# Performance work log

Hardware: AMD Instinct MI355X
Metric: run time of the kernel (lower is better)

Reference implementation:

```python
import jax, jax.numpy as jnp
import numpy as np

D_MODEL = 1024
N_HEADS = 16
D_HEAD = D_MODEL // N_HEADS  # 64
M = int(round(D_HEAD * np.log(D_HEAD)))  # 266 random features, per source
KERNEL_EPS = 1e-4


def setup_inputs() -> dict:
    key = jax.random.key(0)
    ks = jax.random.split(key, 12)
    B, L = 2, 2048
    sc = 1.0 / np.sqrt(D_MODEL)
    return {
        "query": jax.random.normal(ks[0], (B, L, D_MODEL), jnp.float32),
        "key_": jax.random.normal(ks[1], (B, L, D_MODEL), jnp.float32),
        "value": jax.random.normal(ks[2], (B, L, D_MODEL), jnp.float32),
        "Wq": jax.random.normal(ks[3], (D_MODEL, D_MODEL), jnp.float32) * sc,
        "bq": jnp.zeros((D_MODEL,), jnp.float32),
        "Wk": jax.random.normal(ks[4], (D_MODEL, D_MODEL), jnp.float32) * sc,
        "bk": jnp.zeros((D_MODEL,), jnp.float32),
        "Wv": jax.random.normal(ks[5], (D_MODEL, D_MODEL), jnp.float32) * sc,
        "bv": jnp.zeros((D_MODEL,), jnp.float32),
        "Wo": jax.random.normal(ks[6], (D_MODEL, D_MODEL), jnp.float32) * sc,
        "bo": jnp.zeros((D_MODEL,), jnp.float32),
        "random_features": jax.random.normal(ks[7], (M, D_HEAD), jnp.float32),
    }


def _split_heads(x):
    # [B,L,d_model] -> [B,H,L,D]
    B, L, _ = x.shape
    return x.reshape(B, L, N_HEADS, D_HEAD).transpose(0, 2, 1, 3)


def _favor_projected(q, k, rf):
    # q,k: [B,H,L,D]; rf: [M,D]. Faithful to get_projected_queries_and_keys (kernel_type='exp').
    q = q / (D_MODEL ** 0.25)
    k = k / (D_MODEL ** 0.25)
    pq = jnp.einsum('bhld,md->bhlm', q, rf)
    pk = jnp.einsum('bhld,md->bhlm', k, rf)
    h_q = -0.5 * jnp.sum(q * q, axis=-1, keepdims=True)  # [B,H,L,1]
    h_k = -0.5 * jnp.sum(k * k, axis=-1, keepdims=True)
    q_stab = jnp.max(h_q, axis=-1, keepdims=True)  # == h_q (last dim is 1), as in source
    k_stab = jnp.max(h_k)  # global scalar, as in source
    q_ker = jnp.exp(h_q + (pq - q_stab))
    k_ker = jnp.exp(h_k + (pk - k_stab))
    c = M ** (-0.5)
    return c * (q_ker + KERNEL_EPS), c * (k_ker + KERNEL_EPS)


def _causal_favor(qp, kp, v):
    # qp,kp: [L,B,H,M]; v: [L,B,H,D]. Prefix-sum linear attention.
    # Denominator: q_prime[i] . cumsum(k_prime)[i]
    denom = jnp.einsum('lbhm,lbhm->lbh', qp, jnp.cumsum(kp, axis=0))

    # Numerator: recurrent scan carrying S = sum_j k'_j v_j^T  ([B,H,M,D])
    def step(S, inp):
        q_t, k_t, v_t = inp
        S = S + k_t[..., :, None] * v_t[..., None, :]
        out_t = jnp.einsum('bhmd,bhm->bhd', S, q_t)
        return S, out_t

    S0 = jnp.zeros(kp.shape[1:] + (v.shape[-1],), kp.dtype)
    _, num = jax.lax.scan(step, S0, (qp, kp, v))  # num: [L,B,H,D]
    return num / denom[..., None]


def reference(query, key_, value, Wq, bq, Wk, bk, Wv, bv, Wo, bo, random_features):
    B, L, _ = query.shape
    q = _split_heads(query @ Wq + bq)   # [B,H,L,D]
    k = _split_heads(key_ @ Wk + bk)
    v = _split_heads(value @ Wv + bv)
    q_prime, k_prime = _favor_projected(q, k, random_features)  # [B,H,L,M]
    # Causal path operates sequence-first: [L,B,H,*]
    qp = q_prime.transpose(2, 0, 1, 3)
    kp = k_prime.transpose(2, 0, 1, 3)
    vt = v.transpose(2, 0, 1, 3)
    out = _causal_favor(qp, kp, vt)               # [L,B,H,D]
    ctx = out.transpose(1, 0, 2, 3).reshape(B, L, D_MODEL)
    return ctx @ Wo + bo
```

## Files before the change

kernel.cpp:

```cpp
#include <hip/hip_runtime.h>
#include <hip/hip_bf16.h>

#define BATCH 2
#define SEQ 2048
#define DMODEL 1024
#define NH 16
#define HD 64
#define NRF 266
#define NRFP 288
#define SROW 320
#define CHK 128
#define NCH 16
#define NBH 32
#define NROWS 4096

constexpr float SCAL = 0.17677669529663687f;
constexpr float SCAL2 = 0.03125f;
constexpr float LN_CNORM = -2.7917480361965505f;
constexpr float CKEPS = 6.131393094576169e-6f;

typedef short bf16x8 __attribute__((ext_vector_type(8)));
typedef float f32x4 __attribute__((ext_vector_type(4)));

__device__ __forceinline__ short f2bs(float v) {
  __hip_bfloat16 h = __float2bfloat16(v);
  return *reinterpret_cast<short*>(&h);
}
__device__ __forceinline__ float bs2f(short s) {
  __hip_bfloat16 h;
  *reinterpret_cast<short*>(&h) = s;
  return __bfloat162float(h);
}
__device__ __forceinline__ void gload_lds16(const void* g, void* l) {
  __builtin_amdgcn_global_load_lds(
      (const __attribute__((address_space(1))) void*)g,
      (__attribute__((address_space(3))) void*)l, 16, 0, 0);
}
__device__ __forceinline__ unsigned f2ord(float f) {
  unsigned u = __float_as_uint(f);
  return (u & 0x80000000u) ? ~u : (u | 0x80000000u);
}
__device__ __forceinline__ float ord2f(unsigned e) {
  return (e & 0x80000000u) ? __uint_as_float(e & 0x7fffffffu)
                           : __uint_as_float(~e);
}

__global__ __launch_bounds__(256) void cvt3_kernel(const float* __restrict__ q,
                                                   const float* __restrict__ k,
                                                   const float* __restrict__ v,
                                                   short* __restrict__ out) {
  int z = blockIdx.y;
  const float* x = (z == 0) ? q : (z == 1) ? k : v;
  short* y = out + (size_t)z * NROWS * DMODEL;
  int i = (blockIdx.x * 256 + threadIdx.x) * 8;
  float4 a = *(const float4*)&x[i];
  float4 b = *(const float4*)&x[i + 4];
  bf16x8 o;
  o[0] = f2bs(a.x); o[1] = f2bs(a.y); o[2] = f2bs(a.z); o[3] = f2bs(a.w);
  o[4] = f2bs(b.x); o[5] = f2bs(b.y); o[6] = f2bs(b.z); o[7] = f2bs(b.w);
  *(bf16x8*)&y[i] = o;
}

__global__ __launch_bounds__(256) void rf_pad_bf16(const float* __restrict__ rf,
                                                   short* __restrict__ rfb,
                                                   unsigned* __restrict__ kord) {
  int idx = blockIdx.x * 256 + threadIdx.x;
  rfb[idx] = (idx < NRF * HD) ? f2bs(rf[idx] * SCAL) : (short)0;
  if (idx == 0) *kord = 0u;
}

__global__ __launch_bounds__(256) void transpose4_bf16(
    const float* __restrict__ Wq, const float* __restrict__ Wk,
    const float* __restrict__ Wv, const float* __restrict__ Wo,
    short* __restrict__ WtBase) {
  __shared__ float t[32][33];
  int z = blockIdx.z;
  const float* W = (z == 0) ? Wq : (z == 1) ? Wk : (z == 2) ? Wv : Wo;
  short* Wt = WtBase + (size_t)z * DMODEL * DMODEL;
  int k0 = blockIdx.y << 5, n0 = blockIdx.x << 5;
  int tx = threadIdx.x & 31, ty = threadIdx.x >> 5;
#pragma unroll
  for (int rr = 0; rr < 4; ++rr) {
    int r = ty + (rr << 3);
    t[r][tx] = W[(size_t)(k0 + r) * DMODEL + n0 + tx];
  }
  __syncthreads();
#pragma unroll
  for (int rr = 0; rr < 4; ++rr) {
    int r = ty + (rr << 3);
    Wt[(size_t)(n0 + r) * DMODEL + k0 + tx] = f2bs(t[tx][r]);
  }
}

template <bool OUTBF>
__device__ __forceinline__ void gemm_core128(const short* __restrict__ A,
                                             const short* __restrict__ Bt,
                                             const float* __restrict__ bias,
                                             void* __restrict__ C, int bm, int bn) {
  __shared__ short As[2][128 * 64];
  __shared__ short Bs[2][128 * 64];
  int tid = threadIdx.x;
  int lane = tid & 63, wid = tid >> 6;
  int wr = wid >> 1, wc = wid & 1;
  int cl = lane & 15, rq = lane >> 4;
  f32x4 acc[4][4];
#pragma unroll
  for (int m = 0; m < 4; ++m)
#pragma unroll
    for (int n = 0; n < 4; ++n) acc[m][n] = f32x4{0.f, 0.f, 0.f, 0.f};

  auto stage = [&](int buf, int k0) {
#pragma unroll
    for (int i = 0; i < 4; ++i) {
      int e = tid * 8 + i * 2048;
      int row = e >> 6;
      int k = (e & 63) ^ ((row & 7) << 3);
      gload_lds16(A + (size_t)(bm + row) * DMODEL + k0 + k,
                  &As[buf][wid * 512 + i * 2048]);
    }
#pragma unroll
    for (int i = 0; i < 4; ++i) {
      int e = tid * 8 + i * 2048;
      int row = e >> 6;
      int k = (e & 63) ^ ((row & 7) << 3);
      gload_lds16(Bt + (size_t)(bn + row) * DMODEL + k0 + k,
                  &Bs[buf][wid * 512 + i * 2048]);
    }
  };

  stage(0, 0);
#pragma unroll 2
  for (int t = 0; t < 16; ++t) {
    int cur = t & 1;
    if (t < 15) {
      stage(cur ^ 1, (t + 1) * 64);
      asm volatile("s_waitcnt vmcnt(8)" ::: "memory");
    } else {
      asm volatile("s_waitcnt vmcnt(0)" ::: "memory");
    }
    __builtin_amdgcn_s_barrier();
    asm volatile("" ::: "memory");
    const short* curA = &As[cur][0];
    const short* curB = &Bs[cur][0];
#pragma unroll
    for (int ks = 0; ks < 2; ++ks) {
      int kb = ks * 32 + (rq << 3);
      bf16x8 af[4], bfv[4];
#pragma unroll
      for (int mf = 0; mf < 4; ++mf) {
        int row = wr * 64 + mf * 16 + cl;
        af[mf] = *(const bf16x8*)&curA[row * 64 + (kb ^ ((row & 7) << 3))];
      }
#pragma unroll
      for (int nf = 0; nf < 4; ++nf) {
        int row = wc * 64 + nf * 16 + cl;
        bfv[nf] = *(const bf16x8*)&curB[row * 64 + (kb ^ ((row & 7) << 3))];
      }
#pragma unroll
      for (int mf = 0; mf < 4; ++mf)
#pragma unroll
        for (int nf = 0; nf < 4; ++nf)
          acc[mf][nf] = __builtin_amdgcn_mfma_f32_16x16x32_bf16(af[mf], bfv[nf],
                                                                acc[mf][nf], 0, 0, 0);
    }
    __builtin_amdgcn_s_barrier();
    asm volatile("" ::: "memory");
  }
  int rbase = bm + wr * 64 + (rq << 2);
  int cbase = bn + wc * 64 + cl;
#pragma unroll
  for (int nf = 0; nf < 4; ++nf) {
    int col = cbase + nf * 16;
    float bv = bias[col];
#pragma unroll
    for (int mf = 0; mf < 4; ++mf)
#pragma unroll
      for (int r = 0; r < 4; ++r) {
        int row = rbase + mf * 16 + r;
        float v = acc[mf][nf][r] + bv;
        if (OUTBF)
          ((short*)C)[(size_t)row * DMODEL + col] = f2bs(v);
        else
          ((float*)C)[(size_t)row * DMODEL + col] = v;
      }
  }
}

template <bool OUTBF>
__device__ __forceinline__ void gemm_core64(const short* __restrict__ A,
                                            const short* __restrict__ Bt,
                                            const float* __restrict__ bias,
                                            void* __restrict__ C, int bm, int bn) {
  __shared__ short As[2][128 * 64];
  __shared__ short Bs[2][64 * 64];
  int tid = threadIdx.x;
  int lane = tid & 63, wid = tid >> 6;
  int wr = wid >> 1, wc = wid & 1;
  f32x4 acc[4][2];
#pragma unroll
  for (int m = 0; m < 4; ++m)
#pragma unroll
    for (int n = 0; n < 2; ++n) acc[m][n] = f32x4{0.f, 0.f, 0.f, 0.f};

  auto stage = [&](int buf, int k0) {
#pragma unroll
    for (int i = 0; i < 4; ++i) {
      int e = tid * 8 + i * 2048;
      int row = e >> 6;
      int k = (e & 63) ^ ((row & 7) << 3);
      gload_lds16(A + (size_t)(bm + row) * DMODEL + k0 + k,
                  &As[buf][wid * 512 + i * 2048]);
    }
#pragma unroll
    for (int i = 0; i < 2; ++i) {
      int e = tid * 8 + i * 2048;
      int row = e >> 6;
      int k = (e & 63) ^ ((row & 7) << 3);
      gload_lds16(Bt + (size_t)(bn + row) * DMODEL + k0 + k,
                  &Bs[buf][wid * 512 + i * 2048]);
    }
  };

  stage(0, 0);
#pragma unroll 2
  for (int t = 0; t < 16; ++t) {
    int cur = t & 1;
    if (t < 15) {
      stage(cur ^ 1, (t + 1) * 64);
      asm volatile("s_waitcnt vmcnt(6)" ::: "memory");
    } else {
      asm volatile("s_waitcnt vmcnt(0)" ::: "memory");
    }
    __builtin_amdgcn_s_barrier();
    asm volatile("" ::: "memory");
    const short* curA = &As[cur][0];
    const short* curB = &Bs[cur][0];
#pragma unroll
    for (int ks = 0; ks < 2; ++ks) {
      int kb = ks * 32 + ((lane >> 4) << 3);
      bf16x8 af[4], bfv[2];
#pragma unroll
      for (int mf = 0; mf < 4; ++mf) {
        int row = wr * 64 + mf * 16 + (lane & 15);
        af[mf] = *(const bf16x8*)&curA[row * 64 + (kb ^ ((row & 7) << 3))];
      }
#pragma unroll
      for (int nf = 0; nf < 2; ++nf) {
        int row = wc * 32 + nf * 16 + (lane & 15);
        bfv[nf] = *(const bf16x8*)&curB[row * 64 + (kb ^ ((row & 7) << 3))];
      }
#pragma unroll
      for (int mf = 0; mf < 4; ++mf)
#pragma unroll
        for (int nf = 0; nf < 2; ++nf)
          acc[mf][nf] = __builtin_amdgcn_mfma_f32_16x16x32_bf16(af[mf], bfv[nf],
                                                                acc[mf][nf], 0, 0, 0);
    }
    __builtin_amdgcn_s_barrier();
    asm volatile("" ::: "memory");
  }
  int rbase = bm + wr * 64 + ((lane >> 4) << 2);
  int cbase = bn + wc * 32 + (lane & 15);
#pragma unroll
  for (int nf = 0; nf < 2; ++nf) {
    int col = cbase + nf * 16;
    float bv = bias[col];
#pragma unroll
    for (int mf = 0; mf < 4; ++mf)
#pragma unroll
      for (int r = 0; r < 4; ++r) {
        int row = rbase + mf * 16 + r;
        float v = acc[mf][nf][r] + bv;
        if (OUTBF)
          ((short*)C)[(size_t)row * DMODEL + col] = f2bs(v);
        else
          ((float*)C)[(size_t)row * DMODEL + col] = v;
      }
  }
}

__global__ __launch_bounds__(256) void gemm_qkv3(
    const short* __restrict__ Abase, const short* __restrict__ WtBase,
    const float* __restrict__ bq, const float* __restrict__ bk,
    const float* __restrict__ bv, short* __restrict__ OutBase) {
  int z = blockIdx.z;
  const short* A = Abase + (size_t)z * NROWS * DMODEL;
  const short* Bt = WtBase + (size_t)z * DMODEL * DMODEL;
  const float* bias = (z == 0) ? bq : (z == 1) ? bk : bv;
  short* C = OutBase + (size_t)z * NROWS * DMODEL;
  int bid = blockIdx.x + (blockIdx.y << 3);
  int swz = ((bid & 7) << 5) + (bid >> 3);
  int bn = (swz & 7) << 7;
  int bm = (swz >> 3) << 7;
  gemm_core128<true>(A, Bt, bias, C, bm, bn);
}

__global__ __launch_bounds__(256) void gemm_out(const short* __restrict__ A,
                                                const short* __restrict__ Bt,
                                                const float* __restrict__ bias,
                                                float* __restrict__ C) {
  int bid = blockIdx.x + (blockIdx.y << 4);
  int swz = ((bid & 7) << 6) + (bid >> 3);
  int bn = (swz & 15) << 6;
  int bm = (swz >> 4) << 7;
  gemm_core64<false>(A, Bt, bias, C, bm, bn);
}

__global__ __launch_bounds__(256) void hk_kernel(const short* __restrict__ Kb,
                                                 float* __restrict__ hkbuf,
                                                 unsigned* __restrict__ kord) {
  int tid = threadIdx.x;
  int rloc = tid >> 4, h = tid & 15;
  int n = blockIdx.x * 16 + rloc;
  const short* p = Kb + (size_t)n * DMODEL + h * HD;
  float ss = 0.f;
#pragma unroll
  for (int g = 0; g < 8; ++g) {
    bf16x8 v = *(const bf16x8*)(p + g * 8);
#pragma unroll
    for (int e = 0; e < 8; ++e) {
      float x = bs2f(v[e]);
      ss += x * x;
    }
  }
  float hkv = -0.5f * SCAL2 * ss;
  int b = n >> 11, l = n & (SEQ - 1);
  hkbuf[((size_t)(b * NH + h)) * SEQ + l] = hkv;
  __shared__ float red[256];
  red[tid] = hkv;
  __syncthreads();
  for (int s = 128; s > 0; s >>= 1) {
    if (tid < s) red[tid] = fmaxf(red[tid], red[tid + s]);
    __syncthreads();
  }
  if (tid == 0) atomicMax(kord, f2ord(red[0]));
}

__global__ __launch_bounds__(256, 1) void featmap_mfma(
    const short* __restrict__ Qproj, const short* __restrict__ Kproj,
    const short* __restrict__ rfb, const float* __restrict__ hkbuf,
    const unsigned* __restrict__ kord, short* __restrict__ Qp,
    short* __restrict__ Kp) {
  __shared__ short smem[26624];
  __shared__ float hks[128];
  short* As = smem;
  short* Bs = smem + 8192;
  int isK = blockIdx.z;
  const short* X = isK ? Kproj : Qproj;
  short* O = isK ? Kp : Qp;
  int bh = blockIdx.y, b = bh >> 4, h = bh & 15;
  int l0 = blockIdx.x << 7;
  int tid = threadIdx.x, lane = tid & 63, wid = tid >> 6;
  int cl = lane & 15, rq = lane >> 4;

#pragma unroll
  for (int i = 0; i < 4; ++i) {
    int e = tid * 8 + i * 2048;
    int row = e >> 6;
    int k = (e & 63) ^ ((row & 7) << 3);
    gload_lds16(X + ((size_t)b * SEQ + l0 + row) * DMODEL + h * HD + k,
                &As[wid * 512 + i * 2048]);
  }
#pragma unroll
  for (int i = 0; i < 9; ++i) {
    int e = tid * 8 + i * 2048;
    int row = e >> 6;
    int k = (e & 63) ^ ((row & 7) << 3);
    gload_lds16(rfb + row * HD + k, &Bs[wid * 512 + i * 2048]);
  }
  if (isK) {
    float ksv = ord2f(*kord);
    if (tid < 128)
      hks[tid] = hkbuf[(size_t)bh * SEQ + l0 + tid] - ksv + LN_CNORM;
  }
  __syncthreads();

  int i0 = wid * 32;
  f32x4 acc[2][18];
#pragma unroll
  for (int m = 0; m < 2; ++m)
#pragma unroll
    for (int n = 0; n < 18; ++n) acc[m][n] = f32x4{0.f, 0.f, 0.f, 0.f};
#pragma unroll
  for (int ks = 0; ks < 2; ++ks) {
    int kb = ks * 32 + (rq << 3);
    int swz = (cl & 7) << 3;
    bf16x8 af[2];
#pragma unroll
    for (int mf = 0; mf < 2; ++mf) {
      int row = i0 + mf * 16 + cl;
      af[mf] = *(const bf16x8*)&As[row * 64 + (kb ^ swz)];
    }
#pragma unroll
    for (int nf = 0; nf < 18; ++nf) {
      int brow = nf * 16 + cl;
      bf16x8 bv = *(const bf16x8*)&Bs[brow * 64 + (kb ^ swz)];
#pragma unroll
      for (int mf = 0; mf < 2; ++mf)
        acc[mf][nf] = __builtin_amdgcn_mfma_f32_16x16x32_bf16(af[mf], bv,
                                                              acc[mf][nf], 0, 0, 0);
    }
  }

  short* Ps = smem;
#pragma unroll
  for (int hf = 0; hf < 2; ++hf) {
    __syncthreads();
#pragma unroll
    for (int mf = 0; mf < 2; ++mf)
#pragma unroll
      for (int r = 0; r < 4; ++r) {
        int rl = i0 + mf * 16 + (rq << 2) + r;
        float addk = isK ? hks[rl] : LN_CNORM;
#pragma unroll
        for (int nf2 = 0; nf2 < 9; ++nf2) {
          int m = hf * 144 + nf2 * 16 + cl;
          float v = acc[mf][hf * 9 + nf2][r] + addk;
          float o = (m < NRF) ? (__expf(v) + CKEPS) : 0.f;
          Ps[rl * 152 + nf2 * 16 + cl] = f2bs(o);
        }
      }
    __syncthreads();
#pragma unroll
    for (int it = 0; it < 9; ++it) {
      int idx = tid + it * 256;
      int row = idx / 18, ch = idx - row * 18;
      bf16x8 val = *(const bf16x8*)&Ps[row * 152 + ch * 8];
      *(bf16x8*)&O[((size_t)bh * SEQ + l0 + row) * NRFP + hf * 144 + ch * 8] = val;
    }
  }
}

__global__ __launch_bounds__(256) void chunksum_mfma(
    const short* __restrict__ Kp, const short* __restrict__ Vb,
    short* __restrict__ Sct, float* __restrict__ ksum) {
  constexpr int ST = 70;
  __shared__ short KT[NRFP * ST];
  __shared__ short VT[HD * ST];
  int c = blockIdx.x, bh = blockIdx.y;
  int b = bh >> 4, h = bh & 15;
  int tid = threadIdx.x, lane = tid & 63, wv = tid >> 6;
  int cl = lane & 15, rq = lane >> 4;
  int irow = tid >> 2;
  int mq = tid & 3;
  size_t rowb = (size_t)bh * SEQ + (size_t)c * CHK;

  f32x4 acc[18];
#pragma unroll
  for (int m = 0; m < 18; ++m) acc[m] = f32x4{0.f, 0.f, 0.f, 0.f};
  float k1 = 0.f, k2 = 0.f;

  for (int hf = 0; hf < 2; ++hf) {
    __syncthreads();
    const short* Krow = Kp + (rowb + hf * 64 + irow) * NRFP;
#pragma unroll
    for (int cg = 0; cg < 9; ++cg) {
      int m0 = cg * 32 + mq * 8;
      bf16x8 v = *(const bf16x8*)(Krow + m0);
#pragma unroll
      for (int e = 0; e < 8; ++e) KT[(m0 + e) * ST + irow] = v[e];
    }
    const short* Vrow =
        Vb + ((size_t)b * SEQ + (size_t)c * CHK + hf * 64 + irow) * DMODEL + h * HD;
    {
      int d0 = mq * 16;
      bf16x8 v0 = *(const bf16x8*)(Vrow + d0);
      bf16x8 v1 = *(const bf16x8*)(Vrow + d0 + 8);
#pragma unroll
      for (int e = 0; e < 8; ++e) VT[(d0 + e) * ST + irow] = v0[e];
#pragma unroll
      for (int e = 0; e < 8; ++e) VT[(d0 + 8 + e) * ST + irow] = v1[e];
    }
    __syncthreads();
#pragma unroll
    for (int ks = 0; ks < 2; ++ks) {
      int kb = ks * 32 + rq * 8;
      bf16x8 bv = *(const bf16x8*)&VT[(wv * 16 + cl) * ST + kb];
#pragma unroll
      for (int mf = 0; mf < 18; ++mf) {
        bf16x8 av = *(const bf16x8*)&KT[(mf * 16 + cl) * ST + kb];
        acc[mf] = __builtin_amdgcn_mfma_f32_16x16x32_bf16(av, bv, acc[mf], 0, 0, 0);
      }
    }
    {
      const short* r1 = &KT[tid * ST];
#pragma unroll
      for (int g = 0; g < 8; ++g) {
        bf16x8 v = *(const bf16x8*)(r1 + g * 8);
#pragma unroll
        for (int e = 0; e < 8; ++e) k1 += bs2f(v[e]);
      }
      if (tid < 10) {
        const short* r2 = &KT[(256 + tid) * ST];
#pragma unroll
        for (int g = 0; g < 8; ++g) {
          bf16x8 v = *(const bf16x8*)(r2 + g * 8);
#pragma unroll
          for (int e = 0; e < 8; ++e) k2 += bs2f(v[e]);
        }
      }
    }
  }
  size_t sbase = ((size_t)bh * NCH + c) * (size_t)(HD * SROW);
  int d = wv * 16 + cl;
#pragma unroll
  for (int mf = 0; mf < 18; ++mf) {
    short4 o4 = make_short4(f2bs(acc[mf][0]), f2bs(acc[mf][1]),
                            f2bs(acc[mf][2]), f2bs(acc[mf][3]));
    *(short4*)&Sct[sbase + (size_t)d * SROW + mf * 16 + rq * 4] = o4;
  }
  {
    int dz = tid >> 2, off = NRFP + ((tid & 3) << 3);
    bf16x8 z = {0, 0, 0, 0, 0, 0, 0, 0};
    *(bf16x8*)&Sct[sbase + (size_t)dz * SROW + off] = z;
  }
  size_t kbase = ((size_t)bh * NCH + c) * (size_t)NRF;
  if (tid < NRF) ksum[kbase + tid] = k1;
  if (tid < 10) ksum[kbase + 256 + tid] = k2;
}

__global__ __launch_bounds__(256) void prefix_all(const short* __restrict__ Sct,
                                                  short* __restrict__ Spt,
                                                  const float* __restrict__ ksum,
                                                  short* __restrict__ ksb) {
  int bh = blockIdx.y;
  if (blockIdx.x == 80) {
    for (int m = threadIdx.x; m < NRFP; m += 256) {
      if (m < NRF) {
        size_t base = (size_t)bh * NCH * NRF + m;
        float a = 0.f;
#pragma unroll
        for (int c = 0; c < NCH; ++c) {
          float v = ksum[base + (size_t)c * NRF];
          ksb[((size_t)bh * NCH + c) * NRFP + m] = f2bs(a);
          a += v;
        }
      } else {
#pragma unroll
        for (int c = 0; c < NCH; ++c)
          ksb[((size_t)bh * NCH + c) * NRFP + m] = 0;
      }
    }
    return;
  }
  int e = blockIdx.x * 256 + threadIdx.x;
  float a = 0.f;
#pragma unroll
  for (int c = 0; c < NCH; ++c) {
    size_t idx = ((size_t)bh * NCH + c) * (size_t)(HD * SROW) + e;
    float v = bs2f(Sct[idx]);
    Spt[idx] = f2bs(a);
    a += v;
  }
}

__global__ __launch_bounds__(256) void attn_mfma(
    const short* __restrict__ Qp, const short* __restrict__ Kp,
    const short* __restrict__ Vb, const short* __restrict__ Spt,
    const short* __restrict__ ksb, short* __restrict__ ctxb) {
  constexpr int PST = 136;
  __shared__ short Vt[64 * PST];
  __shared__ short SP[64 * SROW];
  int c = blockIdx.x, bh = blockIdx.y;
  int b = bh >> 4, h = bh & 15;
  int tid = threadIdx.x, lane = tid & 63, wid = tid >> 6;
  int cl = lane & 15, rq = lane >> 4;
  size_t rowb = (size_t)bh * SEQ + (size_t)c * CHK;

  const short* sg = Spt + ((size_t)bh * NCH + c) * (size_t)(HD * SROW);
#pragma unroll
  for (int i = 0; i < 10; ++i) {
    int o = tid * 8 + i * 2048;
    int d = o / SROW;
    int m = o - d * SROW;
    int ms = m ^ ((d & 7) << 3);
    gload_lds16(sg + (size_t)d * SROW + ms, &SP[wid * 512 + i * 2048]);
  }
  {
    int jj = tid >> 3, d0 = (tid & 7) << 3;
#pragma unroll
    for (int jt = 0; jt < 4; ++jt) {
      int j = jj + jt * 32;
      bf16x8 v = *(const bf16x8*)(Vb + ((size_t)b * SEQ + (size_t)c * CHK + j) * DMODEL +
                                  h * HD + d0);
#pragma unroll
      for (int e = 0; e < 8; ++e) Vt[(d0 + e) * PST + j] = v[e];
    }
  }
  __syncthreads();

  int i0 = wid * 32;
  const short* Arow = Qp + (rowb + i0) * NRFP;
  const short* Krow = Kp + rowb * NRFP;
  const short* krow = ksb + ((size_t)bh * NCH + c) * NRFP;
  f32x4 accI[2][4];
  f32x4 accD[2];
  f32x4 accP[2][8];
#pragma unroll
  for (int m = 0; m < 2; ++m) {
#pragma unroll
    for (int n = 0; n < 4; ++n) accI[m][n] = f32x4{0.f, 0.f, 0.f, 0.f};
    accD[m] = f32x4{0.f, 0.f, 0.f, 0.f};
#pragma unroll
    for (int n = 0; n < 8; ++n) accP[m][n] = f32x4{0.f, 0.f, 0.f, 0.f};
  }
#pragma unroll
  for (int k9 = 0; k9 < 9; ++k9) {
    int kb = k9 * 32 + (rq << 3);
    bf16x8 af[2];
#pragma unroll
    for (int mf = 0; mf < 2; ++mf)
      af[mf] = *(const bf16x8*)(Arow + (size_t)(mf * 16 + cl) * NRFP + kb);
    bf16x8 bvD = {0, 0, 0, 0, 0, 0, 0, 0};
    if (cl == 0) bvD = *(const bf16x8*)(krow + kb);
#pragma unroll
    for (int mf = 0; mf < 2; ++mf)
      accD[mf] = __builtin_amdgcn_mfma_f32_16x16x32_bf16(af[mf], bvD, accD[mf], 0, 0, 0);
#pragma unroll
    for (int nf = 0; nf < 4; ++nf) {
      int row = nf * 16 + cl;
      bf16x8 bv = *(const bf16x8*)&SP[row * SROW + (kb ^ ((cl & 7) << 3))];
#pragma unroll
      for (int mf = 0; mf < 2; ++mf)
        accI[mf][nf] = __builtin_amdgcn_mfma_f32_16x16x32_bf16(af[mf], bv,
                                                               accI[mf][nf], 0, 0, 0);
    }
#pragma unroll
    for (int nf = 0; nf < 8; ++nf) {
      bf16x8 bv = *(const bf16x8*)(Krow + (size_t)(nf * 16 + cl) * NRFP + kb);
#pragma unroll
      for (int mf = 0; mf < 2; ++mf)
        accP[mf][nf] = __builtin_amdgcn_mfma_f32_16x16x32_bf16(af[mf], bv,
                                                               accP[mf][nf], 0, 0, 0);
    }
  }
  __syncthreads();

  float dtot[2][4];
#pragma unroll
  for (int mf = 0; mf < 2; ++mf)
#pragma unroll
    for (int r = 0; r < 4; ++r) {
      int rl = mf * 16 + (rq << 2) + r;
      int row = i0 + rl;
      float dsum = 0.f;
#pragma unroll
      for (int nf = 0; nf < 8; ++nf) {
        int col = nf * 16 + cl;
        float v = (col > row) ? 0.f : accP[mf][nf][r];
        dsum += v;
        SP[wid * 32 * PST + rl * PST + col] = f2bs(v);
      }
      dsum += __shfl_xor(dsum, 1);
      dsum += __shfl_xor(dsum, 2);
      dsum += __shfl_xor(dsum, 4);
      dsum += __shfl_xor(dsum, 8);
      float dden = __shfl(accD[mf][r], lane & 48);
      dtot[mf][r] = dden + dsum;
    }
  __syncthreads();

  f32x4 pacc[2][4];
#pragma unroll
  for (int m = 0; m < 2; ++m)
#pragma unroll
    for (int n = 0; n < 4; ++n) pacc[m][n] = f32x4{0.f, 0.f, 0.f, 0.f};
#pragma unroll
  for (int kk = 0; kk < 4; ++kk) {
    int kb = kk * 32 + (rq << 3);
    bf16x8 paf[2];
#pragma unroll
    for (int mf = 0; mf < 2; ++mf)
      paf[mf] = *(const bf16x8*)&SP[wid * 32 * PST + (mf * 16 + cl) * PST + kb];
#pragma unroll
    for (int nf = 0; nf < 4; ++nf) {
      bf16x8 bv = *(const bf16x8*)&Vt[(nf * 16 + cl) * PST + kb];
#pragma unroll
      for (int mf = 0; mf < 2; ++mf)
        pacc[mf][nf] = __builtin_amdgcn_mfma_f32_16x16x32_bf16(paf[mf], bv,
                                                               pacc[mf][nf], 0, 0, 0);
    }
  }
#pragma unroll
  for (int mf = 0; mf < 2; ++mf)
#pragma unroll
    for (int r = 0; r < 4; ++r) {
      int row = i0 + mf * 16 + (rq << 2) + r;
      float inv = 1.0f / dtot[mf][r];
      size_t ob = ((size_t)b * SEQ + (size_t)c * CHK + row) * DMODEL + h * HD;
#pragma unroll
      for (int nf = 0; nf < 4; ++nf) {
        int d = nf * 16 + cl;
        float v = (accI[mf][nf][r] + pacc[mf][nf][r]) * inv;
        ctxb[ob + d] = f2bs(v);
      }
    }
}

extern "C" void kernel_launch(void* const* d_in, const int* in_sizes, int n_in,
                              void* d_out, int out_size, void* d_ws, size_t ws_size,
                              hipStream_t stream) {
  (void)in_sizes; (void)n_in; (void)out_size;
  const float* query = (const float*)d_in[0];
  const float* key_  = (const float*)d_in[1];
  const float* value = (const float*)d_in[2];
  const float* Wq = (const float*)d_in[3];
  const float* bq = (const float*)d_in[4];
  const float* Wk = (const float*)d_in[5];
  const float* bk = (const float*)d_in[6];
  const float* Wv = (const float*)d_in[7];
  const float* bv = (const float*)d_in[8];
  const float* Wo = (const float*)d_in[9];
  const float* bo = (const float*)d_in[10];
  const float* rf = (const float*)d_in[11];

  constexpr size_t SZ_INBF = (size_t)NROWS * DMODEL * 2;
  constexpr size_t SZ_QP   = (size_t)NBH * SEQ * NRFP * 2;
  constexpr size_t SZ_WT   = (size_t)DMODEL * DMODEL * 2;
  constexpr size_t SZ_SCH  = (size_t)NBH * NCH * HD * SROW * 2;
  constexpr size_t SZ_KS   = (size_t)NBH * NCH * NRF * 4;
  constexpr size_t SZ_KSB  = (size_t)NBH * NCH * NRFP * 2;
  constexpr size_t SZ_HK   = (size_t)NBH * SEQ * 4;
  constexpr size_t SZ_RFB  = (size_t)NRFP * HD * 2;

  constexpr size_t O_QP   = 0;
  constexpr size_t O_KP   = O_QP + SZ_QP;
  constexpr size_t O_WT   = O_KP + SZ_QP;
  constexpr size_t O_QPR  = O_WT + 4 * SZ_WT;
  constexpr size_t O_SCH  = O_QPR + 3 * SZ_INBF;
  constexpr size_t O_SPR  = O_SCH + SZ_SCH;
  constexpr size_t O_KSUM = O_SPR + SZ_SCH;
  constexpr size_t O_KSB  = O_KSUM + SZ_KS;
  constexpr size_t O_HK   = O_KSB + SZ_KSB;
  constexpr size_t O_KST  = O_HK + SZ_HK;
  constexpr size_t O_CTXB = O_KST + 256;
  constexpr size_t O_RFB  = O_CTXB + SZ_INBF;
  constexpr size_t O_END  = O_RFB + SZ_RFB;
  if (ws_size < O_END) return;

  char* w = (char*)d_ws;
  short* Qbf  = (short*)(w + O_QP);
  short* Qp   = (short*)(w + O_QP);
  short* Kp   = (short*)(w + O_KP);
  short* WtB  = (short*)(w + O_WT);
  short* QprB = (short*)(w + O_QPR);
  short* Kpr  = (short*)(w + O_QPR + SZ_INBF);
  short* Vpr  = (short*)(w + O_QPR + 2 * SZ_INBF);
  short* Sct  = (short*)(w + O_SCH);
  short* Spt  = (short*)(w + O_SPR);
  float* ksum = (float*)(w + O_KSUM);
  short* ksb  = (short*)(w + O_KSB);
  float* hkbuf = (float*)(w + O_HK);
  unsigned* kord = (unsigned*)(w + O_KST);
  short* ctxb = (short*)(w + O_CTXB);
  short* rfb  = (short*)(w + O_RFB);

  constexpr int NEL = NROWS * DMODEL;
  cvt3_kernel<<<dim3(NEL / 2048, 3), 256, 0, stream>>>(query, key_, value, Qbf);
  transpose4_bf16<<<dim3(32, 32, 4), 256, 0, stream>>>(Wq, Wk, Wv, Wo, WtB);
  rf_pad_bf16<<<(NRFP * HD) / 256, 256, 0, stream>>>(rf, rfb, kord);
  gemm_qkv3<<<dim3(8, 32, 3), 256, 0, stream>>>(Qbf, WtB, bq, bk, bv, QprB);
  hk_kernel<<<256, 256, 0, stream>>>(Kpr, hkbuf, kord);
  featmap_mfma<<<dim3(SEQ / 128, NBH, 2), 256, 0, stream>>>(QprB, Kpr, rfb, hkbuf,
                                                            kord, Qp, Kp);
  chunksum_mfma<<<dim3(NCH, NBH), 256, 0, stream>>>(Kp, Vpr, Sct, ksum);
  prefix_all<<<dim3(81, NBH), 256, 0, stream>>>(Sct, Spt, ksum, ksb);
  attn_mfma<<<dim3(NCH, NBH), 256, 0, stream>>>(Qp, Kp, Vpr, Spt, ksb, ctxb);
  gemm_out<<<dim3(16, 32), 256, 0, stream>>>(ctxb, WtB + 3 * (size_t)DMODEL * DMODEL,
                                             bo, (float*)d_out);
}
```

Measured before the change: 184.1 us.

## Split attention chunk across two blocks and read prefix state from global

The attention kernel now launches two blocks per chunk, each handling 64 query rows, so the grid doubles from 512 to 1024 blocks and occupancy rises. The upper half skips the causally masked key columns and only computes 64 of the 128 intra-chunk columns. The prefix state is no longer staged into LDS with a swizzle but read directly from global memory per fragment, which lowers LDS use but adds uncached global traffic. Each wave now owns 16 rows instead of 32, so fewer registers are held but operand reuse across row fragments is lost.

Result: slower. 191.0 us (+3.8%).

```diff
diff --git a/kernel.cpp b/kernel.cpp
--- a/kernel.cpp
+++ b/kernel.cpp
@@ -554,147 +554,128 @@
   }
 }
 
+template <int Z>
+__device__ __forceinline__ void attn_body(short* smem, const short* __restrict__ Qp,
+                                          const short* __restrict__ Kp,
+                                          const short* __restrict__ Vb,
+                                          const short* __restrict__ Spt,
+                                          const short* __restrict__ ksb,
+                                          short* __restrict__ ctxb, int c, int bh) {
+  constexpr int JN = Z ? 128 : 64;
+  constexpr int PST = Z ? 136 : 72;
+  constexpr int NPF = Z ? 8 : 4;
+  constexpr int KK = Z ? 4 : 2;
+  short* Vt = smem;
+  short* Pl = smem + 64 * PST;
+  int b = bh >> 4, h = bh & 15;
+  int tid = threadIdx.x, lane = tid & 63, wid = tid >> 6;
+  int cl = lane & 15, rq = lane >> 4;
+  size_t rowb = (size_t)bh * SEQ + (size_t)c * CHK;
+
+  {
+    int jj = tid >> 3, d0 = (tid & 7) << 3;
+#pragma unroll
+    for (int jt = 0; jt < JN / 32; ++jt) {
+      int j = jj + jt * 32;
+      bf16x8 v = *(const bf16x8*)(Vb + ((size_t)b * SEQ + (size_t)c * CHK + j) * DMODEL +
+                                  h * HD + d0);
+#pragma unroll
+      for (int e = 0; e < 8; ++e) Vt[(d0 + e) * PST + j] = v[e];
+    }
+  }
+  __syncthreads();
+
+  int i0 = Z * 64 + wid * 16;
+  const short* Arow = Qp + (rowb + i0) * NRFP;
+  const short* Krow = Kp + rowb * NRFP;
+  const short* SptG = Spt + ((size_t)bh * NCH + c) * (size_t)(HD * SROW);
+  const short* krow = ksb + ((size_t)bh * NCH + c) * NRFP;
+  f32x4 accI[4];
+  f32x4 accD = f32x4{0.f, 0.f, 0.f, 0.f};
+  f32x4 accP[NPF];
+#pragma unroll
+  for (int n = 0; n < 4; ++n) accI[n] = f32x4{0.f, 0.f, 0.f, 0.f};
+#pragma unroll
+  for (int n = 0; n < NPF; ++n) accP[n] = f32x4{0.f, 0.f, 0.f, 0.f};
+
+#pragma unroll
+  for (int k9 = 0; k9 < 9; ++k9) {
+    int kb = k9 * 32 + (rq << 3);
+    bf16x8 af = *(const bf16x8*)(Arow + (size_t)cl * NRFP + kb);
+    bf16x8 bvD = {0, 0, 0, 0, 0, 0, 0, 0};
+    if (cl == 0) bvD = *(const bf16x8*)(krow + kb);
+    accD = __builtin_amdgcn_mfma_f32_16x16x32_bf16(af, bvD, accD, 0, 0, 0);
+#pragma unroll
+    for (int nf = 0; nf < 4; ++nf) {
+      bf16x8 bv = *(const bf16x8*)(SptG + (size_t)(nf * 16 + cl) * SROW + kb);
+      accI[nf] = __builtin_amdgcn_mfma_f32_16x16x32_bf16(af, bv, accI[nf], 0, 0, 0);
+    }
+#pragma unroll
+    for (int nf = 0; nf < NPF; ++nf) {
+      bf16x8 bv = *(const bf16x8*)(Krow + (size_t)(nf * 16 + cl) * NRFP + kb);
+      accP[nf] = __builtin_amdgcn_mfma_f32_16x16x32_bf16(af, bv, accP[nf], 0, 0, 0);
+    }
+  }
+
+  float dtot[4];
+#pragma unroll
+  for (int r = 0; r < 4; ++r) {
+    int rl = (rq << 2) + r;
+    int rowc = i0 + rl;
+    int rowl = wid * 16 + rl;
+    float dsum = 0.f;
+#pragma unroll
+    for (int nf = 0; nf < NPF; ++nf) {
+      int col = nf * 16 + cl;
+      float v = (col > rowc) ? 0.f : accP[nf][r];
+      dsum += v;
+      Pl[rowl * PST + col] = f2bs(v);
+    }
+    dsum += __shfl_xor(dsum, 1);
+    dsum += __shfl_xor(dsum, 2);
+    dsum += __shfl_xor(dsum, 4);
+    dsum += __shfl_xor(dsum, 8);
+    float dden = __shfl(accD[r], lane & 48);
+    dtot[r] = dden + dsum;
+  }
+  __syncthreads();
+
+  f32x4 pacc[4];
+#pragma unroll
+  for (int n = 0; n < 4; ++n) pacc[n] = f32x4{0.f, 0.f, 0.f, 0.f};
+#pragma unroll
+  for (int kk = 0; kk < KK; ++kk) {
+    int kb = kk * 32 + (rq << 3);
+    bf16x8 paf = *(const bf16x8*)&Pl[(wid * 16 + cl) * PST + kb];
+#pragma unroll
+    for (int nf = 0; nf < 4; ++nf) {
+      bf16x8 bv = *(const bf16x8*)&Vt[(nf * 16 + cl) * PST + kb];
+      pacc[nf] = __builtin_amdgcn_mfma_f32_16x16x32_bf16(paf, bv, pacc[nf], 0, 0, 0);
+    }
+  }
+#pragma unroll
+  for (int r = 0; r < 4; ++r) {
+    int rowc = i0 + (rq << 2) + r;
+    float inv = 1.0f / dtot[r];
+    size_t ob = ((size_t)b * SEQ + (size_t)c * CHK + rowc) * DMODEL + h * HD;
+#pragma unroll
+    for (int nf = 0; nf < 4; ++nf) {
+      int d = nf * 16 + cl;
+      ctxb[ob + d] = f2bs((accI[nf][r] + pacc[nf][r]) * inv);
+    }
+  }
+}
+
 __global__ __launch_bounds__(256) void attn_mfma(
     const short* __restrict__ Qp, const short* __restrict__ Kp,
     const short* __restrict__ Vb, const short* __restrict__ Spt,
     const short* __restrict__ ksb, short* __restrict__ ctxb) {
-  constexpr int PST = 136;
-  __shared__ short Vt[64 * PST];
-  __shared__ short SP[64 * SROW];
+  __shared__ short smem[2 * 64 * 136];
   int c = blockIdx.x, bh = blockIdx.y;
-  int b = bh >> 4, h = bh & 15;
-  int tid = threadIdx.x, lane = tid & 63, wid = tid >> 6;
-  int cl = lane & 15, rq = lane >> 4;
-  size_t rowb = (size_t)bh * SEQ + (size_t)c * CHK;
-
-  const short* sg = Spt + ((size_t)bh * NCH + c) * (size_t)(HD * SROW);
-#pragma unroll
-  for (int i = 0; i < 10; ++i) {
-    int o = tid * 8 + i * 2048;
-    int d = o / SROW;
-    int m = o - d * SROW;
-    int ms = m ^ ((d & 7) << 3);
-    gload_lds16(sg + (size_t)d * SROW + ms, &SP[wid * 512 + i * 2048]);
-  }
-  {
-    int jj = tid >> 3, d0 = (tid & 7) << 3;
-#pragma unroll
-    for (int jt = 0; jt < 4; ++jt) {
-      int j = jj + jt * 32;
-      bf16x8 v = *(const bf16x8*)(Vb + ((size_t)b * SEQ + (size_t)c * CHK + j) * DMODEL +
-                                  h * HD + d0);
-#pragma unroll
-      for (int e = 0; e < 8; ++e) Vt[(d0 + e) * PST + j] = v[e];
-    }
-  }
-  __syncthreads();
-
-  int i0 = wid * 32;
-  const short* Arow = Qp + (rowb + i0) * NRFP;
-  const short* Krow = Kp + rowb * NRFP;
-  const short* krow = ksb + ((size_t)bh * NCH + c) * NRFP;
-  f32x4 accI[2][4];
-  f32x4 accD[2];
-  f32x4 accP[2][8];
-#pragma unroll
-  for (int m = 0; m < 2; ++m) {
-#pragma unroll
-    for (int n = 0; n < 4; ++n) accI[m][n] = f32x4{0.f, 0.f, 0.f, 0.f};
-    accD[m] = f32x4{0.f, 0.f, 0.f, 0.f};
-#pragma unroll
-    for (int n = 0; n < 8; ++n) accP[m][n] = f32x4{0.f, 0.f, 0.f, 0.f};
-  }
-#pragma unroll
-  for (int k9 = 0; k9 < 9; ++k9) {
-    int kb = k9 * 32 + (rq << 3);
-    bf16x8 af[2];
-#pragma unroll
-    for (int mf = 0; mf < 2; ++mf)
-      af[mf] = *(const bf16x8*)(Arow + (size_t)(mf * 16 + cl) * NRFP + kb);
-    bf16x8 bvD = {0, 0, 0, 0, 0, 0, 0, 0};
-    if (cl == 0) bvD = *(const bf16x8*)(krow + kb);
-#pragma unroll
-    for (int mf = 0; mf < 2; ++mf)
-      accD[mf] = __builtin_amdgcn_mfma_f32_16x16x32_bf16(af[mf], bvD, accD[mf], 0, 0, 0);
-#pragma unroll
-    for (int nf = 0; nf < 4; ++nf) {
-      int row = nf * 16 + cl;
-      bf16x8 bv = *(const bf16x8*)&SP[row * SROW + (kb ^ ((cl & 7) << 3))];
-#pragma unroll
-      for (int mf = 0; mf < 2; ++mf)
-        accI[mf][nf] = __builtin_amdgcn_mfma_f32_16x16x32_bf16(af[mf], bv,
-                                                               accI[mf][nf], 0, 0, 0);
-    }
-#pragma unroll
-    for (int nf = 0; nf < 8; ++nf) {
-      bf16x8 bv = *(const bf16x8*)(Krow + (size_t)(nf * 16 + cl) * NRFP + kb);
-#pragma unroll
-      for (int mf = 0; mf < 2; ++mf)
-        accP[mf][nf] = __builtin_amdgcn_mfma_f32_16x16x32_bf16(af[mf], bv,
-                                                               accP[mf][nf], 0, 0, 0);
-    }
-  }
-  __syncthreads();
-
-  float dtot[2][4];
-#pragma unroll
-  for (int mf = 0; mf < 2; ++mf)
-#pragma unroll
-    for (int r = 0; r < 4; ++r) {
-      int rl = mf * 16 + (rq << 2) + r;
-      int row = i0 + rl;
-      float dsum = 0.f;
-#pragma unroll
-      for (int nf = 0; nf < 8; ++nf) {
-        int col = nf * 16 + cl;
-        float v = (col > row) ? 0.f : accP[mf][nf][r];
-        dsum += v;
-        SP[wid * 32 * PST + rl * PST + col] = f2bs(v);
-      }
-      dsum += __shfl_xor(dsum, 1);
-      dsum += __shfl_xor(dsum, 2);
-      dsum += __shfl_xor(dsum, 4);
-      dsum += __shfl_xor(dsum, 8);
-      float dden = __shfl(accD[mf][r], lane & 48);
-      dtot[mf][r] = dden + dsum;
-    }
-  __syncthreads();
-
-  f32x4 pacc[2][4];
-#pragma unroll
-  for (int m = 0; m < 2; ++m)
-#pragma unroll
-    for (int n = 0; n < 4; ++n) pacc[m][n] = f32x4{0.f, 0.f, 0.f, 0.f};
-#pragma unroll
-  for (int kk = 0; kk < 4; ++kk) {
-    int kb = kk * 32 + (rq << 3);
-    bf16x8 paf[2];
-#pragma unroll
-    for (int mf = 0; mf < 2; ++mf)
-      paf[mf] = *(const bf16x8*)&SP[wid * 32 * PST + (mf * 16 + cl) * PST + kb];
-#pragma unroll
-    for (int nf = 0; nf < 4; ++nf) {
-      bf16x8 bv = *(const bf16x8*)&Vt[(nf * 16 + cl) * PST + kb];
-#pragma unroll
-      for (int mf = 0; mf < 2; ++mf)
-        pacc[mf][nf] = __builtin_amdgcn_mfma_f32_16x16x32_bf16(paf[mf], bv,
-                                                               pacc[mf][nf], 0, 0, 0);
-    }
-  }
-#pragma unroll
-  for (int mf = 0; mf < 2; ++mf)
-#pragma unroll
-    for (int r = 0; r < 4; ++r) {
-      int row = i0 + mf * 16 + (rq << 2) + r;
-      float inv = 1.0f / dtot[mf][r];
-      size_t ob = ((size_t)b * SEQ + (size_t)c * CHK + row) * DMODEL + h * HD;
-#pragma unroll
-      for (int nf = 0; nf < 4; ++nf) {
-        int d = nf * 16 + cl;
-        float v = (accI[mf][nf][r] + pacc[mf][nf][r]) * inv;
-        ctxb[ob + d] = f2bs(v);
-      }
-    }
+  if (blockIdx.z == 0)
+    attn_body<0>(smem, Qp, Kp, Vb, Spt, ksb, ctxb, c, bh);
+  else
+    attn_body<1>(smem, Qp, Kp, Vb, Spt, ksb, ctxb, c, bh);
 }
 
 extern "C" void kernel_launch(void* const* d_in, const int* in_sizes, int n_in,
@@ -765,7 +746,7 @@
                                                             kord, Qp, Kp);
   chunksum_mfma<<<dim3(NCH, NBH), 256, 0, stream>>>(Kp, Vpr, Sct, ksum);
   prefix_all<<<dim3(81, NBH), 256, 0, stream>>>(Sct, Spt, ksum, ksb);
-  attn_mfma<<<dim3(NCH, NBH), 256, 0, stream>>>(Qp, Kp, Vpr, Spt, ksb, ctxb);
+  attn_mfma<<<dim3(NCH, NBH, 2), 256, 0, stream>>>(Qp, Kp, Vpr, Spt, ksb, ctxb);
   gemm_out<<<dim3(16, 32), 256, 0, stream>>>(ctxb, WtB + 3 * (size_t)DMODEL * DMODEL,
                                              bo, (float*)d_out);
 }
```

## Double-buffer K-prime tiles in LDS for the intra-chunk attention MFMA loop

Applied to the files above, without the earlier changes.

The attention kernel previously read K-prime B-operand fragments for the intra-chunk QK^T product directly from global memory, with all four waves fetching the same rows. These reads are replaced with a double-buffered LDS staging scheme: async global-to-LDS loads of 128x32 tiles with an XOR swizzle, prefetch of the next k-slice, vmcnt waits and barriers each iteration. The V transpose load is moved ahead of the S-prefix load so the waits line up. This aims to cut redundant global traffic and hide latency, at the cost of extra LDS, two barriers per iteration and a loop that is no longer fully unrolled.

After: 171.3 us. -7.0%, faster.

```diff
diff --git a/kernel.cpp b/kernel.cpp
--- a/kernel.cpp
+++ b/kernel.cpp
@@ -561,12 +561,24 @@
   constexpr int PST = 136;
   __shared__ short Vt[64 * PST];
   __shared__ short SP[64 * SROW];
+  __shared__ short Kb2[2][128 * 32];
   int c = blockIdx.x, bh = blockIdx.y;
   int b = bh >> 4, h = bh & 15;
   int tid = threadIdx.x, lane = tid & 63, wid = tid >> 6;
   int cl = lane & 15, rq = lane >> 4;
   size_t rowb = (size_t)bh * SEQ + (size_t)c * CHK;
 
+  {
+    int jj = tid >> 3, d0 = (tid & 7) << 3;
+#pragma unroll
+    for (int jt = 0; jt < 4; ++jt) {
+      int j = jj + jt * 32;
+      bf16x8 v = *(const bf16x8*)(Vb + ((size_t)b * SEQ + (size_t)c * CHK + j) * DMODEL +
+                                  h * HD + d0);
+#pragma unroll
+      for (int e = 0; e < 8; ++e) Vt[(d0 + e) * PST + j] = v[e];
+    }
+  }
   const short* sg = Spt + ((size_t)bh * NCH + c) * (size_t)(HD * SROW);
 #pragma unroll
   for (int i = 0; i < 10; ++i) {
@@ -576,22 +588,21 @@
     int ms = m ^ ((d & 7) << 3);
     gload_lds16(sg + (size_t)d * SROW + ms, &SP[wid * 512 + i * 2048]);
   }
-  {
-    int jj = tid >> 3, d0 = (tid & 7) << 3;
-#pragma unroll
-    for (int jt = 0; jt < 4; ++jt) {
-      int j = jj + jt * 32;
-      bf16x8 v = *(const bf16x8*)(Vb + ((size_t)b * SEQ + (size_t)c * CHK + j) * DMODEL +
-                                  h * HD + d0);
-#pragma unroll
-      for (int e = 0; e < 8; ++e) Vt[(d0 + e) * PST + j] = v[e];
-    }
-  }
-  __syncthreads();
+  const short* Kbase = Kp + rowb * NRFP;
+  auto stageK = [&](int buf, int k0) {
+#pragma unroll
+    for (int i = 0; i < 2; ++i) {
+      int chunk = tid + i * 256;
+      int row = chunk >> 2, cc = chunk & 3;
+      int col = k0 + ((cc ^ (row & 3)) << 3);
+      gload_lds16(Kbase + (size_t)row * NRFP + col,
+                  &Kb2[buf][(wid * 64 + i * 256) * 8]);
+    }
+  };
+  stageK(0, 0);
 
   int i0 = wid * 32;
   const short* Arow = Qp + (rowb + i0) * NRFP;
-  const short* Krow = Kp + rowb * NRFP;
   const short* krow = ksb + ((size_t)bh * NCH + c) * NRFP;
   f32x4 accI[2][4];
   f32x4 accD[2];
@@ -604,8 +615,16 @@
 #pragma unroll
     for (int n = 0; n < 8; ++n) accP[m][n] = f32x4{0.f, 0.f, 0.f, 0.f};
   }
-#pragma unroll
   for (int k9 = 0; k9 < 9; ++k9) {
+    int cur = k9 & 1;
+    if (k9 < 8) {
+      stageK(cur ^ 1, (k9 + 1) * 32);
+      asm volatile("s_waitcnt vmcnt(2)" ::: "memory");
+    } else {
+      asm volatile("s_waitcnt vmcnt(0)" ::: "memory");
+    }
+    __builtin_amdgcn_s_barrier();
+    asm volatile("" ::: "memory");
     int kb = k9 * 32 + (rq << 3);
     bf16x8 af[2];
 #pragma unroll
@@ -625,16 +644,19 @@
         accI[mf][nf] = __builtin_amdgcn_mfma_f32_16x16x32_bf16(af[mf], bv,
                                                                accI[mf][nf], 0, 0, 0);
     }
+    const short* kcur = &Kb2[cur][0];
 #pragma unroll
     for (int nf = 0; nf < 8; ++nf) {
-      bf16x8 bv = *(const bf16x8*)(Krow + (size_t)(nf * 16 + cl) * NRFP + kb);
+      int row = nf * 16 + cl;
+      bf16x8 bv = *(const bf16x8*)&kcur[row * 32 + ((rq ^ (cl & 3)) << 3)];
 #pragma unroll
       for (int mf = 0; mf < 2; ++mf)
         accP[mf][nf] = __builtin_amdgcn_mfma_f32_16x16x32_bf16(af[mf], bv,
                                                                accP[mf][nf], 0, 0, 0);
     }
-  }
-  __syncthreads();
+    __builtin_amdgcn_s_barrier();
+    asm volatile("" ::: "memory");
+  }
 
   float dtot[2][4];
 #pragma unroll
```
